# Kernel optimization log

Measured on AMD Instinct MI355X. Metric: run time of the kernel, lower is better.

## Reference

```python
import jax, jax.numpy as jnp
import numpy as np

N_NODES = 100000
N_INCID = 2000000
HIDDEN = 128
N_HE = 100000


def setup_inputs() -> dict:
    key = jax.random.key(0)
    k1, k2, k3 = jax.random.split(key, 3)
    node_feats = jax.random.normal(k1, (N_NODES, HIDDEN), dtype=jnp.float32)
    hyperedge_index = jax.random.randint(k2, (2, N_INCID), 0, N_HE, dtype=jnp.int64)
    # xavier_uniform for Linear(hidden,1): bound = sqrt(6/(hidden+1))
    bound = float(np.sqrt(6.0 / (HIDDEN + 1)))
    W = jax.random.uniform(k3, (1, HIDDEN), dtype=jnp.float32, minval=-bound, maxval=bound)
    return {"node_feats": node_feats, "hyperedge_index": hyperedge_index,
            "num_hyperedges": N_HE, "W": W}


def reference(node_feats, hyperedge_index, num_hyperedges, W):
    node_idx = hyperedge_index[0]
    he_idx = hyperedge_index[1]
    gathered = node_feats[node_idx]                      # [E, D]
    scores = jnp.einsum('ed,d->e', gathered, W[0])       # [E]
    # segment softmax over hyperedges
    seg_max = jax.ops.segment_max(scores, he_idx, num_segments=num_hyperedges)
    seg_max = jnp.where(jnp.isfinite(seg_max), seg_max, 0.0)  # empty segments
    w = jnp.exp(scores - seg_max[he_idx])                # [E]
    denom = jax.ops.segment_sum(w, he_idx, num_segments=num_hyperedges)
    w_norm = w / jnp.maximum(denom, 1e-20)[he_idx]       # [E]
    # weighted scatter-sum; empty hyperedges stay zero
    out = jax.ops.segment_sum(w_norm[:, None] * gathered, he_idx,
                              num_segments=num_hyperedges)  # [H, D]
    return out
```

## Files before the change

kernel.cpp:

```cpp
#include <hip/hip_runtime.h>
#include <hip/hip_fp16.h>
#include <math.h>

#define N_NODES 100000
#define N_INCID 2000000
#define HIDDEN  128
#define N_HE    100000

#define EPB 1024
#define FILL_BLOCKS ((N_INCID + EPB - 1) / EPB)
#define PREP_BLOCKS ((N_NODES + 3) / 4)

__device__ inline float4 h4_to_f4(uint2 p) {
    __half2 a = *(__half2*)&p.x;
    __half2 b = *(__half2*)&p.y;
    float2 fa = __half22float2(a);
    float2 fb = __half22float2(b);
    return make_float4(fa.x, fa.y, fb.x, fb.y);
}

__global__ void prep_fill_kernel(const float* __restrict__ nf,
                                 const float* __restrict__ W,
                                 const int* __restrict__ idx,
                                 float* __restrict__ en,
                                 __half2* __restrict__ nfh2,
                                 int* __restrict__ head,
                                 int2* __restrict__ next8) {
    int b = blockIdx.x;
    if (b < FILL_BLOCKS) {
        int base = b * EPB;
        int e = base + threadIdx.x;
        if (base + EPB <= N_INCID) {
            int he[4], nd[4], prev[4];
            #pragma unroll
            for (int k = 0; k < 4; ++k) {
                he[k] = idx[N_INCID + e + 256 * k];
                nd[k] = idx[e + 256 * k];
            }
            #pragma unroll
            for (int k = 0; k < 4; ++k)
                prev[k] = atomicExch(&head[he[k]], e + 256 * k);
            #pragma unroll
            for (int k = 0; k < 4; ++k)
                next8[e + 256 * k] = make_int2(nd[k], prev[k]);
        } else {
            #pragma unroll
            for (int k = 0; k < 4; ++k) {
                int ek = e + 256 * k;
                if (ek < N_INCID) {
                    int he = idx[N_INCID + ek];
                    int nd = idx[ek];
                    int prev = atomicExch(&head[he], ek);
                    next8[ek] = make_int2(nd, prev);
                }
            }
        }
    } else {
        int wave = threadIdx.x >> 6, lane = threadIdx.x & 63;
        int n = (b - FILL_BLOCKS) * 4 + wave;
        if (n >= N_NODES) return;
        const float2* nf2 = (const float2*)nf;
        const float2* w2  = (const float2*)W;
        float2 v = nf2[(size_t)n * 64 + lane];
        float2 w = w2[lane];
        float p = v.x * w.x + v.y * w.y;
        #pragma unroll
        for (int o = 32; o > 0; o >>= 1) p += __shfl_xor(p, o, 64);
        if (lane == 0) en[n] = __expf(p);
        nfh2[(size_t)n * 64 + lane] = __floats2half2_rn(v.x, v.y);
    }
}

__global__ void compute_kernel_h(const int* __restrict__ head,
                                 const int2* __restrict__ next8,
                                 const float* __restrict__ en,
                                 const uint2* __restrict__ nfh4,
                                 float* __restrict__ out) {
    int wave = threadIdx.x >> 6, lane = threadIdx.x & 63;
    int half = lane >> 5, l32 = lane & 31;
    int he = blockIdx.x * 8 + wave * 2 + half;
    if (he >= N_HE) return;

    float4 acc = make_float4(0.f, 0.f, 0.f, 0.f);
    float denom = 0.f;
    int e = head[he];
    while (e >= 0) {
        int2 p = next8[e];
        float w = en[p.x];
        float4 v = h4_to_f4(nfh4[(size_t)p.x * 32 + l32]);
        acc.x += w * v.x; acc.y += w * v.y;
        acc.z += w * v.z; acc.w += w * v.w;
        denom += w;
        e = p.y;
    }
    float inv = 1.0f / fmaxf(denom, 1e-20f);
    acc.x *= inv; acc.y *= inv; acc.z *= inv; acc.w *= inv;
    ((float4*)out)[(size_t)he * 32 + l32] = acc;
}

extern "C" void kernel_launch(void* const* d_in, const int* in_sizes, int n_in,
                              void* d_out, int out_size, void* d_ws, size_t ws_size,
                              hipStream_t stream) {
    const float* nf  = (const float*)d_in[0];
    const int*   idx = (const int*)d_in[1];
    const float* W   = (const float*)d_in[3];
    float* out = (float*)d_out;
    char* ws = (char*)d_ws;

    int*     head  = (int*)(ws + 0);
    float*   en    = (float*)(ws + 400000);
    __half2* nfh2  = (__half2*)(ws + 800000);
    int2*    next8 = (int2*)(ws + 26400000);

    hipMemsetAsync(head, 0xFF, N_HE * sizeof(int), stream);
    prep_fill_kernel<<<FILL_BLOCKS + PREP_BLOCKS, 256, 0, stream>>>(
        nf, W, idx, en, nfh2, head, next8);
    compute_kernel_h<<<(N_HE + 7) / 8, 256, 0, stream>>>(
        head, next8, en, (const uint2*)nfh2, out);
}
```

Before: 330.9 us.

## Split hyperedge linked lists into four chains and walk them concurrently

Each hyperedge's incidence linked list is split into four independent chains, keyed by the incidence index mod 4. The compute kernel walks all four chains at once, so several dependent pointer-chasing loads are in flight per iteration. One wave now handles one hyperedge, with each lane owning one half2 instead of half a wave owning a float4. The fill and prep blocks are interleaved across the grid so atomic-heavy fill work and streaming prep work run together. The costs are a head array four times larger plus its memset, branchier loop code, and a longer critical path where chains are uneven.

```diff
diff --git a/kernel.cpp b/kernel.cpp
--- a/kernel.cpp
+++ b/kernel.cpp
@@ -10,14 +10,7 @@
 #define EPB 1024
 #define FILL_BLOCKS ((N_INCID + EPB - 1) / EPB)
 #define PREP_BLOCKS ((N_NODES + 3) / 4)
-
-__device__ inline float4 h4_to_f4(uint2 p) {
-    __half2 a = *(__half2*)&p.x;
-    __half2 b = *(__half2*)&p.y;
-    float2 fa = __half22float2(a);
-    float2 fb = __half22float2(b);
-    return make_float4(fa.x, fa.y, fb.x, fb.y);
-}
+#define GRID (FILL_BLOCKS + PREP_BLOCKS)
 
 __global__ void prep_fill_kernel(const float* __restrict__ nf,
                                  const float* __restrict__ W,
@@ -27,8 +20,10 @@
                                  int* __restrict__ head,
                                  int2* __restrict__ next8) {
     int b = blockIdx.x;
-    if (b < FILL_BLOCKS) {
-        int base = b * EPB;
+    int fills_before = (int)(((long long)b * FILL_BLOCKS) / GRID);
+    int fills_incl   = (int)(((long long)(b + 1) * FILL_BLOCKS) / GRID);
+    if (fills_incl > fills_before) {
+        int base = fills_before * EPB;
         int e = base + threadIdx.x;
         if (base + EPB <= N_INCID) {
             int he[4], nd[4], prev[4];
@@ -38,8 +33,10 @@
                 nd[k] = idx[e + 256 * k];
             }
             #pragma unroll
-            for (int k = 0; k < 4; ++k)
-                prev[k] = atomicExch(&head[he[k]], e + 256 * k);
+            for (int k = 0; k < 4; ++k) {
+                int ek = e + 256 * k;
+                prev[k] = atomicExch(&head[(ek & 3) * N_HE + he[k]], ek);
+            }
             #pragma unroll
             for (int k = 0; k < 4; ++k)
                 next8[e + 256 * k] = make_int2(nd[k], prev[k]);
@@ -48,16 +45,17 @@
             for (int k = 0; k < 4; ++k) {
                 int ek = e + 256 * k;
                 if (ek < N_INCID) {
-                    int he = idx[N_INCID + ek];
+                    int h = idx[N_INCID + ek];
                     int nd = idx[ek];
-                    int prev = atomicExch(&head[he], ek);
+                    int prev = atomicExch(&head[(ek & 3) * N_HE + h], ek);
                     next8[ek] = make_int2(nd, prev);
                 }
             }
         }
     } else {
+        int pb = b - fills_before;
         int wave = threadIdx.x >> 6, lane = threadIdx.x & 63;
-        int n = (b - FILL_BLOCKS) * 4 + wave;
+        int n = pb * 4 + wave;
         if (n >= N_NODES) return;
         const float2* nf2 = (const float2*)nf;
         const float2* w2  = (const float2*)W;
@@ -74,28 +72,52 @@
 __global__ void compute_kernel_h(const int* __restrict__ head,
                                  const int2* __restrict__ next8,
                                  const float* __restrict__ en,
-                                 const uint2* __restrict__ nfh4,
+                                 const unsigned int* __restrict__ nfh1,
                                  float* __restrict__ out) {
     int wave = threadIdx.x >> 6, lane = threadIdx.x & 63;
-    int half = lane >> 5, l32 = lane & 31;
-    int he = blockIdx.x * 8 + wave * 2 + half;
+    int he = blockIdx.x * 4 + wave;
     if (he >= N_HE) return;
 
-    float4 acc = make_float4(0.f, 0.f, 0.f, 0.f);
+    int e0 = head[he];
+    int e1 = head[N_HE + he];
+    int e2 = head[2 * N_HE + he];
+    int e3 = head[3 * N_HE + he];
+    float2 acc = make_float2(0.f, 0.f);
     float denom = 0.f;
-    int e = head[he];
-    while (e >= 0) {
-        int2 p = next8[e];
-        float w = en[p.x];
-        float4 v = h4_to_f4(nfh4[(size_t)p.x * 32 + l32]);
-        acc.x += w * v.x; acc.y += w * v.y;
-        acc.z += w * v.z; acc.w += w * v.w;
-        denom += w;
-        e = p.y;
+
+    while ((e0 >= 0) || (e1 >= 0) || (e2 >= 0) || (e3 >= 0)) {
+        int n0 = -1, n1 = -1, n2 = -1, n3 = -1;
+        if (e0 >= 0) { int2 p = next8[e0]; n0 = p.x; e0 = p.y; }
+        if (e1 >= 0) { int2 p = next8[e1]; n1 = p.x; e1 = p.y; }
+        if (e2 >= 0) { int2 p = next8[e2]; n2 = p.x; e2 = p.y; }
+        if (e3 >= 0) { int2 p = next8[e3]; n3 = p.x; e3 = p.y; }
+        if (n0 >= 0) {
+            float w = en[n0];
+            unsigned int q = nfh1[(size_t)n0 * 64 + lane];
+            float2 f = __half22float2(*(__half2*)&q);
+            acc.x += w * f.x; acc.y += w * f.y; denom += w;
+        }
+        if (n1 >= 0) {
+            float w = en[n1];
+            unsigned int q = nfh1[(size_t)n1 * 64 + lane];
+            float2 f = __half22float2(*(__half2*)&q);
+            acc.x += w * f.x; acc.y += w * f.y; denom += w;
+        }
+        if (n2 >= 0) {
+            float w = en[n2];
+            unsigned int q = nfh1[(size_t)n2 * 64 + lane];
+            float2 f = __half22float2(*(__half2*)&q);
+            acc.x += w * f.x; acc.y += w * f.y; denom += w;
+        }
+        if (n3 >= 0) {
+            float w = en[n3];
+            unsigned int q = nfh1[(size_t)n3 * 64 + lane];
+            float2 f = __half22float2(*(__half2*)&q);
+            acc.x += w * f.x; acc.y += w * f.y; denom += w;
+        }
     }
     float inv = 1.0f / fmaxf(denom, 1e-20f);
-    acc.x *= inv; acc.y *= inv; acc.z *= inv; acc.w *= inv;
-    ((float4*)out)[(size_t)he * 32 + l32] = acc;
+    ((float2*)out)[(size_t)he * 64 + lane] = make_float2(acc.x * inv, acc.y * inv);
 }
 
 extern "C" void kernel_launch(void* const* d_in, const int* in_sizes, int n_in,
@@ -108,13 +130,12 @@
     char* ws = (char*)d_ws;
 
     int*     head  = (int*)(ws + 0);
-    float*   en    = (float*)(ws + 400000);
-    __half2* nfh2  = (__half2*)(ws + 800000);
-    int2*    next8 = (int2*)(ws + 26400000);
+    float*   en    = (float*)(ws + 1600000);
+    __half2* nfh2  = (__half2*)(ws + 2000000);
+    int2*    next8 = (int2*)(ws + 27600000);
 
-    hipMemsetAsync(head, 0xFF, N_HE * sizeof(int), stream);
-    prep_fill_kernel<<<FILL_BLOCKS + PREP_BLOCKS, 256, 0, stream>>>(
-        nf, W, idx, en, nfh2, head, next8);
-    compute_kernel_h<<<(N_HE + 7) / 8, 256, 0, stream>>>(
-        head, next8, en, (const uint2*)nfh2, out);
+    hipMemsetAsync(head, 0xFF, 4 * N_HE * sizeof(int), stream);
+    prep_fill_kernel<<<GRID, 256, 0, stream>>>(nf, W, idx, en, nfh2, head, next8);
+    compute_kernel_h<<<(N_HE + 3) / 4, 256, 0, stream>>>(
+        head, next8, en, (const unsigned int*)nfh2, out);
 }
```

New measurement: 396.9 us. +19.9%, slower.
